# Kernel tuning notes

Hardware: AMD Instinct MI355X
Metric: run time of the kernel (lower is better)

The kernel has to match this reference:

```python
import jax, jax.numpy as jnp
import numpy as np

C = 512
CQK = C // 8  # 64


def setup_inputs() -> dict:
    key = jax.random.key(0)
    ks = jax.random.split(key, 8)
    B, H, W = 16, 32, 32
    x = jax.random.normal(ks[0], (B, C, H, W), dtype=jnp.float32)
    # 1x1 conv weights stored as [out_ch, in_ch] matrices + biases
    sq = 1.0 / np.sqrt(C)
    Wq = jax.random.uniform(ks[1], (CQK, C), jnp.float32, -sq, sq)
    bq = jax.random.uniform(ks[2], (CQK,), jnp.float32, -sq, sq)
    Wk = jax.random.uniform(ks[3], (CQK, C), jnp.float32, -sq, sq)
    bk = jax.random.uniform(ks[4], (CQK,), jnp.float32, -sq, sq)
    Wv = jax.random.uniform(ks[5], (C, C), jnp.float32, -sq, sq)
    bv = jax.random.uniform(ks[6], (C,), jnp.float32, -sq, sq)
    gamma = jax.random.normal(ks[7], (1,), dtype=jnp.float32)
    return {"x": x, "Wq": Wq, "bq": bq, "Wk": Wk, "bk": bk, "Wv": Wv, "bv": bv, "gamma": gamma}


def reference(x, Wq, bq, Wk, bk, Wv, bv, gamma):
    B, Cin, H, W = x.shape
    xf = x.reshape(B, Cin, H * W)  # [B, C, N]
    # 1x1 convs == channel matmuls
    q = jnp.einsum('qc,bcn->bnq', Wq, xf) + bq[None, None, :]   # [B, N, Cqk]
    k = jnp.einsum('qc,bcn->bqn', Wk, xf) + bk[None, :, None]   # [B, Cqk, N]
    v = jnp.einsum('vc,bcn->bvn', Wv, xf) + bv[None, :, None]   # [B, C, N]
    scores = jnp.einsum('bnq,bqm->bnm', q, k)                    # [B, N, N]
    attn = jax.nn.softmax(scores, axis=-1)                       # softmax over keys
    # values @ attn^T : out[b,c,n] = sum_m v[b,c,m] * attn[b,n,m]
    attended = jnp.einsum('bvm,bnm->bvn', v, attn)               # [B, C, N]
    attended = attended.reshape(B, Cin, H, W)
    return gamma[0] * attended + x
```

## Files before the change

### kernel.cpp

```cpp
#include <hip/hip_runtime.h>
#include <stdint.h>

#define BB 16
#define CC 512
#define CQK 64
#define NN 1024

typedef __attribute__((ext_vector_type(8))) short bf16x8;
typedef __attribute__((ext_vector_type(4))) short short4v;
typedef __attribute__((ext_vector_type(8))) unsigned short ushort8;
typedef __attribute__((ext_vector_type(4))) float f32x4;

static __device__ __forceinline__ unsigned short f2bf(float f) {
  uint32_t u = __float_as_uint(f);
  u += 0x7FFFu + ((u >> 16) & 1u);
  return (unsigned short)(u >> 16);
}

static __device__ __forceinline__ void gll16(const unsigned short* g, unsigned short* l) {
  const __attribute__((address_space(1))) unsigned int* gp =
      reinterpret_cast<const __attribute__((address_space(1))) unsigned int*>(
          reinterpret_cast<uintptr_t>(g));
  __attribute__((address_space(3))) unsigned int* lp =
      reinterpret_cast<__attribute__((address_space(3))) unsigned int*>(
          (unsigned int)reinterpret_cast<uintptr_t>(l));
  __builtin_amdgcn_global_load_lds(gp, lp, 16, 0, 0);
}

__global__ __launch_bounds__(256) void k_pack_w(
    const float* __restrict__ Wq, const float* __restrict__ Wk,
    const float* __restrict__ Wv, unsigned short* __restrict__ Wall) {
  int idx = blockIdx.x * 256 + threadIdx.x;
  int e = idx * 4;
  if (e >= 640 * 512) return;
  int o = e >> 9;
  int c = e & 511;
  const float* src;
  if (o < 64)        src = Wq + (size_t)o * 512;
  else if (o < 128)  src = Wk + (size_t)(o - 64) * 512;
  else               src = Wv + (size_t)(o - 128) * 512;
  float4 v = *(const float4*)(src + c);
  short4v pk;
  pk[0] = (short)f2bf(v.x); pk[1] = (short)f2bf(v.y);
  pk[2] = (short)f2bf(v.z); pk[3] = (short)f2bf(v.w);
  *(short4v*)(Wall + e) = pk;
}

__global__ __launch_bounds__(256) void k_transpose_x(
    const float* __restrict__ x, unsigned short* __restrict__ xT) {
  __shared__ float tile[32][33];
  int b = blockIdx.z;
  int c0 = blockIdx.y * 32;
  int n0 = blockIdx.x * 32;
  int t = threadIdx.x;
  int tn = t & 31, tc = t >> 5;
  const float* xp = x + ((size_t)b * CC + c0) * NN + n0;
#pragma unroll
  for (int i = 0; i < 4; i++) {
    int c = tc + i * 8;
    tile[c][tn] = xp[(size_t)c * NN + tn];
  }
  __syncthreads();
  unsigned short* xq = xT + ((size_t)b * NN + n0) * CC + c0;
  int n = t >> 3;
  int cq = (t & 7) * 4;
  short4v pk;
#pragma unroll
  for (int k = 0; k < 4; k++) pk[k] = (short)f2bf(tile[cq + k][n]);
  *(short4v*)(&xq[(size_t)n * CC + cq]) = pk;
}

__global__ __launch_bounds__(256) void k_gemm1(
    const unsigned short* __restrict__ Wall, const unsigned short* __restrict__ xT,
    const float* __restrict__ bq, const float* __restrict__ bk,
    const float* __restrict__ bv,
    unsigned short* __restrict__ qkT, unsigned short* __restrict__ vbuf) {
  __shared__ __align__(16) unsigned short ldsA[128 * 32];
  __shared__ __align__(16) unsigned short ldsB[128 * 32];
  int b = blockIdx.z;
  int o0 = blockIdx.y * 128;
  int n0 = blockIdx.x * 128;
  int t = threadIdx.x;
  int w = t >> 6, l = t & 63;
  int wm = w & 1, wn = w >> 1;
  int lr = l & 15, lq = l >> 4;

  f32x4 acc[4][4];
#pragma unroll
  for (int i = 0; i < 4; i++)
#pragma unroll
    for (int j = 0; j < 4; j++) acc[i][j] = (f32x4){0.f, 0.f, 0.f, 0.f};

  const unsigned short* Ab = Wall + (size_t)o0 * CC;
  const unsigned short* Bb = xT + ((size_t)b * NN + n0) * CC;
  int srow = t >> 2;
  int skq = (t & 3) * 8;
  int ldsw = (t >> 6) * 512;

  for (int kt = 0; kt < CC; kt += 32) {
#pragma unroll
    for (int p = 0; p < 2; p++) {
      int r = p * 64 + srow;
      gll16(&Ab[(size_t)r * CC + kt + skq], &ldsA[p * 2048 + ldsw]);
      gll16(&Bb[(size_t)r * CC + kt + skq], &ldsB[p * 2048 + ldsw]);
    }
    __syncthreads();
    bf16x8 af[4], bfr[4];
#pragma unroll
    for (int i = 0; i < 4; i++)
      af[i] = *(const bf16x8*)(&ldsA[(wm * 64 + i * 16 + lr) * 32 + lq * 8]);
#pragma unroll
    for (int j = 0; j < 4; j++)
      bfr[j] = *(const bf16x8*)(&ldsB[(wn * 64 + j * 16 + lr) * 32 + lq * 8]);
#pragma unroll
    for (int i = 0; i < 4; i++)
#pragma unroll
      for (int j = 0; j < 4; j++)
        acc[i][j] = __builtin_amdgcn_mfma_f32_16x16x32_bf16(af[i], bfr[j], acc[i][j], 0, 0, 0);
    __syncthreads();
  }

  if (o0 == 0) {
#pragma unroll
    for (int i = 0; i < 4; i++) {
      int ob = wm * 64 + i * 16 + lq * 4;
#pragma unroll
      for (int j = 0; j < 4; j++) {
        int n = n0 + wn * 64 + j * 16 + lr;
        short4v pk;
#pragma unroll
        for (int r = 0; r < 4; r++) {
          int o = ob + r;
          float bias = (o < 64) ? bq[o] : bk[o - 64];
          pk[r] = (short)f2bf(acc[i][j][r] + bias);
        }
        *(short4v*)(&qkT[((size_t)b * NN + n) * 128 + ob]) = pk;
      }
    }
  } else {
#pragma unroll
    for (int i = 0; i < 4; i++) {
#pragma unroll
      for (int r = 0; r < 4; r++) {
        int o = o0 + wm * 64 + i * 16 + lq * 4 + r;
        int c = o - 128;
        float bias = bv[c];
#pragma unroll
        for (int j = 0; j < 4; j++) {
          int n = n0 + wn * 64 + j * 16 + lr;
          vbuf[((size_t)b * CC + c) * NN + n] = f2bf(acc[i][j][r] + bias);
        }
      }
    }
  }
}

#define QT 64
#define MC 64
#define PSTR 72

__global__ __launch_bounds__(256, 4) void k_flash(
    const unsigned short* __restrict__ qkT, const unsigned short* __restrict__ vbuf,
    const float* __restrict__ x, const float* __restrict__ gamma,
    float* __restrict__ out) {
  __shared__ __align__(16) unsigned short P[2][QT * PSTR];
  __shared__ float red[4 * QT];
  __shared__ float fin[QT];

  int lin = blockIdx.x;
  int ntile = lin >> 6;
  int rem = lin & 63;
  int b = rem >> 2;
  int cq = rem & 3;
  int n0 = ntile * QT;
  int t = threadIdx.x;
  int w = t >> 6, l = t & 63;
  int lr = l & 15, lq = l >> 4;
  const unsigned short* qk = qkT + (size_t)b * NN * 128;
  const unsigned short* Vb = vbuf + ((size_t)b * CC + cq * 128 + w * 32) * NN;

  bf16x8 aq[4][2];
#pragma unroll
  for (int nj = 0; nj < 4; nj++)
#pragma unroll
    for (int ks = 0; ks < 2; ks++)
      aq[nj][ks] = *(const bf16x8*)(&qk[(size_t)(n0 + nj * 16 + lr) * 128 + ks * 32 + lq * 8]);

  f32x4 acc[2][4];
#pragma unroll
  for (int ci = 0; ci < 2; ci++)
#pragma unroll
    for (int nj = 0; nj < 4; nj++) acc[ci][nj] = (f32x4){0.f, 0.f, 0.f, 0.f};
  float sreg[4][4];
#pragma unroll
  for (int nj = 0; nj < 4; nj++)
#pragma unroll
    for (int r = 0; r < 4; r++) sreg[nj][r] = 0.f;

  float ev[4][4];
  {
    int mrow = w * 16 + lr;
    bf16x8 kf0 = *(const bf16x8*)(&qk[(size_t)mrow * 128 + 64 + lq * 8]);
    bf16x8 kf1 = *(const bf16x8*)(&qk[(size_t)mrow * 128 + 96 + lq * 8]);
#pragma unroll
    for (int nj = 0; nj < 4; nj++) {
      f32x4 s = (f32x4){0.f, 0.f, 0.f, 0.f};
      s = __builtin_amdgcn_mfma_f32_16x16x32_bf16(aq[nj][0], kf0, s, 0, 0, 0);
      s = __builtin_amdgcn_mfma_f32_16x16x32_bf16(aq[nj][1], kf1, s, 0, 0, 0);
#pragma unroll
      for (int r = 0; r < 4; r++) {
        float e = __expf(s[r]);
        ev[nj][r] = e;
        sreg[nj][r] += e;
      }
    }
  }

  for (int ch = 0; ch < NN / MC; ch++) {
    int m0 = ch * MC;
    unsigned short* Pb = P[ch & 1];
#pragma unroll
    for (int nj = 0; nj < 4; nj++)
#pragma unroll
      for (int r = 0; r < 4; r++)
        Pb[(nj * 16 + lq * 4 + r) * PSTR + w * 16 + lr] = f2bf(ev[nj][r]);

    if (ch + 1 < NN / MC) {
      int mrow = m0 + MC + w * 16 + lr;
      bf16x8 kf0 = *(const bf16x8*)(&qk[(size_t)mrow * 128 + 64 + lq * 8]);
      bf16x8 kf1 = *(const bf16x8*)(&qk[(size_t)mrow * 128 + 96 + lq * 8]);
#pragma unroll
      for (int nj = 0; nj < 4; nj++) {
        f32x4 s = (f32x4){0.f, 0.f, 0.f, 0.f};
        s = __builtin_amdgcn_mfma_f32_16x16x32_bf16(aq[nj][0], kf0, s, 0, 0, 0);
        s = __builtin_amdgcn_mfma_f32_16x16x32_bf16(aq[nj][1], kf1, s, 0, 0, 0);
#pragma unroll
        for (int r = 0; r < 4; r++) {
          float e = __expf(s[r]);
          ev[nj][r] = e;
          sreg[nj][r] += e;
        }
      }
    }

    bf16x8 af[2][2];
#pragma unroll
    for (int ci = 0; ci < 2; ci++)
#pragma unroll
      for (int ks = 0; ks < 2; ks++)
        af[ci][ks] = *(const bf16x8*)(&Vb[(size_t)(ci * 16 + lr) * NN + m0 + ks * 32 + lq * 8]);

    __syncthreads();

#pragma unroll
    for (int ks = 0; ks < 2; ks++)
#pragma unroll
      for (int nj = 0; nj < 4; nj++) {
        bf16x8 pf = *(const bf16x8*)(&Pb[(nj * 16 + lr) * PSTR + ks * 32 + lq * 8]);
#pragma unroll
        for (int ci = 0; ci < 2; ci++)
          acc[ci][nj] = __builtin_amdgcn_mfma_f32_16x16x32_bf16(af[ci][ks], pf, acc[ci][nj], 0, 0, 0);
      }
  }

#pragma unroll
  for (int nj = 0; nj < 4; nj++)
#pragma unroll
    for (int r = 0; r < 4; r++) {
#pragma unroll
      for (int d = 1; d < 16; d <<= 1) sreg[nj][r] += __shfl_xor(sreg[nj][r], d, 64);
    }
  __syncthreads();
  if (lr == 0) {
#pragma unroll
    for (int nj = 0; nj < 4; nj++)
#pragma unroll
      for (int r = 0; r < 4; r++) red[w * QT + nj * 16 + lq * 4 + r] = sreg[nj][r];
  }
  __syncthreads();
  if (t < QT) {
    fin[t] = red[t] + red[QT + t] + red[2 * QT + t] + red[3 * QT + t];
  }
  __syncthreads();

  float invL[4];
#pragma unroll
  for (int nj = 0; nj < 4; nj++) invL[nj] = 1.0f / fin[nj * 16 + lr];
  float g = gamma[0];
#pragma unroll
  for (int ci = 0; ci < 2; ci++) {
#pragma unroll
    for (int r = 0; r < 4; r++) {
      int c = cq * 128 + w * 32 + ci * 16 + lq * 4 + r;
#pragma unroll
      for (int nj = 0; nj < 4; nj++) {
        size_t idx = ((size_t)b * CC + c) * NN + n0 + nj * 16 + lr;
        out[idx] = g * acc[ci][nj][r] * invL[nj] + x[idx];
      }
    }
  }
}

extern "C" void kernel_launch(void* const* d_in, const int* in_sizes, int n_in,
                              void* d_out, int out_size, void* d_ws, size_t ws_size,
                              hipStream_t stream) {
  (void)in_sizes; (void)n_in; (void)out_size; (void)ws_size;
  const float* x     = (const float*)d_in[0];
  const float* Wq    = (const float*)d_in[1];
  const float* bq    = (const float*)d_in[2];
  const float* Wk    = (const float*)d_in[3];
  const float* bk    = (const float*)d_in[4];
  const float* Wv    = (const float*)d_in[5];
  const float* bv    = (const float*)d_in[6];
  const float* gamma = (const float*)d_in[7];
  float* out = (float*)d_out;

  char* ws = (char*)d_ws;
  unsigned short* Wall = (unsigned short*)(ws);
  unsigned short* xT   = (unsigned short*)(ws + 655360);
  unsigned short* qkT  = (unsigned short*)(ws + 655360 + 16777216);
  unsigned short* vbuf = (unsigned short*)(ws + 655360 + 16777216 + 4194304);

  k_pack_w<<<dim3(320), dim3(256), 0, stream>>>(Wq, Wk, Wv, Wall);
  k_transpose_x<<<dim3(NN / 32, CC / 32, BB), dim3(256), 0, stream>>>(x, xT);
  k_gemm1<<<dim3(NN / 128, 640 / 128, BB), dim3(256), 0, stream>>>(Wall, xT, bq, bk, bv, qkT, vbuf);
  k_flash<<<dim3((NN / QT) * 4 * BB), dim3(256), 0, stream>>>(qkT, vbuf, x, gamma, out);
}
```

Measured before the change: 184.0 us.

## Merge prep kernels and widen flash block to 512 threads over half channels

Merges the weight packing and x transpose into a single launch to cut one kernel launch. The flash kernel now uses 8 waves per block, each block covering half the channels instead of a quarter. It processes 128 keys per chunk, so each block computes scores for a query tile once for twice as many channels, halving redundant QK/softmax work. V loads are hoisted ahead of the next-chunk score computation. The trade-off is more registers and more LDS per block, plus fewer blocks in the grid.

```diff
diff --git a/kernel.cpp b/kernel.cpp
--- a/kernel.cpp
+++ b/kernel.cpp
@@ -27,47 +27,49 @@
   __builtin_amdgcn_global_load_lds(gp, lp, 16, 0, 0);
 }
 
-__global__ __launch_bounds__(256) void k_pack_w(
-    const float* __restrict__ Wq, const float* __restrict__ Wk,
-    const float* __restrict__ Wv, unsigned short* __restrict__ Wall) {
-  int idx = blockIdx.x * 256 + threadIdx.x;
-  int e = idx * 4;
-  if (e >= 640 * 512) return;
-  int o = e >> 9;
-  int c = e & 511;
-  const float* src;
-  if (o < 64)        src = Wq + (size_t)o * 512;
-  else if (o < 128)  src = Wk + (size_t)(o - 64) * 512;
-  else               src = Wv + (size_t)(o - 128) * 512;
-  float4 v = *(const float4*)(src + c);
-  short4v pk;
-  pk[0] = (short)f2bf(v.x); pk[1] = (short)f2bf(v.y);
-  pk[2] = (short)f2bf(v.z); pk[3] = (short)f2bf(v.w);
-  *(short4v*)(Wall + e) = pk;
-}
-
-__global__ __launch_bounds__(256) void k_transpose_x(
-    const float* __restrict__ x, unsigned short* __restrict__ xT) {
-  __shared__ float tile[32][33];
-  int b = blockIdx.z;
-  int c0 = blockIdx.y * 32;
-  int n0 = blockIdx.x * 32;
+__global__ __launch_bounds__(256) void k_prep(
+    const float* __restrict__ x, const float* __restrict__ Wq,
+    const float* __restrict__ Wk, const float* __restrict__ Wv,
+    unsigned short* __restrict__ xT, unsigned short* __restrict__ Wall) {
+  int blk = blockIdx.x;
   int t = threadIdx.x;
-  int tn = t & 31, tc = t >> 5;
-  const float* xp = x + ((size_t)b * CC + c0) * NN + n0;
-#pragma unroll
-  for (int i = 0; i < 4; i++) {
-    int c = tc + i * 8;
-    tile[c][tn] = xp[(size_t)c * NN + tn];
-  }
-  __syncthreads();
-  unsigned short* xq = xT + ((size_t)b * NN + n0) * CC + c0;
-  int n = t >> 3;
-  int cq = (t & 7) * 4;
-  short4v pk;
-#pragma unroll
-  for (int k = 0; k < 4; k++) pk[k] = (short)f2bf(tile[cq + k][n]);
-  *(short4v*)(&xq[(size_t)n * CC + cq]) = pk;
+  if (blk < 8192) {
+    __shared__ float tile[32][33];
+    int b = blk >> 9;
+    int rem = blk & 511;
+    int c0 = (rem >> 5) * 32;
+    int n0 = (rem & 31) * 32;
+    int tn = t & 31, tc = t >> 5;
+    const float* xp = x + ((size_t)b * CC + c0) * NN + n0;
+#pragma unroll
+    for (int i = 0; i < 4; i++) {
+      int c = tc + i * 8;
+      tile[c][tn] = xp[(size_t)c * NN + tn];
+    }
+    __syncthreads();
+    unsigned short* xq = xT + ((size_t)b * NN + n0) * CC + c0;
+    int n = t >> 3;
+    int cq = (t & 7) * 4;
+    short4v pk;
+#pragma unroll
+    for (int k = 0; k < 4; k++) pk[k] = (short)f2bf(tile[cq + k][n]);
+    *(short4v*)(&xq[(size_t)n * CC + cq]) = pk;
+  } else {
+    int idx = (blk - 8192) * 256 + t;
+    int e = idx * 4;
+    if (e >= 640 * 512) return;
+    int o = e >> 9;
+    int c = e & 511;
+    const float* src;
+    if (o < 64)        src = Wq + (size_t)o * 512;
+    else if (o < 128)  src = Wk + (size_t)(o - 64) * 512;
+    else               src = Wv + (size_t)(o - 128) * 512;
+    float4 v = *(const float4*)(src + c);
+    short4v pk;
+    pk[0] = (short)f2bf(v.x); pk[1] = (short)f2bf(v.y);
+    pk[2] = (short)f2bf(v.z); pk[3] = (short)f2bf(v.w);
+    *(short4v*)(Wall + e) = pk;
+  }
 }
 
 __global__ __launch_bounds__(256) void k_gemm1(
@@ -156,28 +158,28 @@
 }
 
 #define QT 64
-#define MC 64
-#define PSTR 72
-
-__global__ __launch_bounds__(256, 4) void k_flash(
+#define MC 128
+#define PSTR 136
+
+__global__ __launch_bounds__(512, 4) void k_flash(
     const unsigned short* __restrict__ qkT, const unsigned short* __restrict__ vbuf,
     const float* __restrict__ x, const float* __restrict__ gamma,
     float* __restrict__ out) {
   __shared__ __align__(16) unsigned short P[2][QT * PSTR];
-  __shared__ float red[4 * QT];
+  __shared__ float red[8 * QT];
   __shared__ float fin[QT];
 
   int lin = blockIdx.x;
-  int ntile = lin >> 6;
-  int rem = lin & 63;
-  int b = rem >> 2;
-  int cq = rem & 3;
+  int ntile = lin >> 5;
+  int rem = lin & 31;
+  int b = rem >> 1;
+  int chalf = rem & 1;
   int n0 = ntile * QT;
   int t = threadIdx.x;
   int w = t >> 6, l = t & 63;
   int lr = l & 15, lq = l >> 4;
   const unsigned short* qk = qkT + (size_t)b * NN * 128;
-  const unsigned short* Vb = vbuf + ((size_t)b * CC + cq * 128 + w * 32) * NN;
+  const unsigned short* Vb = vbuf + ((size_t)b * CC + chalf * 256 + w * 32) * NN;
 
   bf16x8 aq[4][2];
 #pragma unroll
@@ -225,15 +227,25 @@
       for (int r = 0; r < 4; r++)
         Pb[(nj * 16 + lq * 4 + r) * PSTR + w * 16 + lr] = f2bf(ev[nj][r]);
 
+    bf16x8 kf0n, kf1n;
     if (ch + 1 < NN / MC) {
       int mrow = m0 + MC + w * 16 + lr;
-      bf16x8 kf0 = *(const bf16x8*)(&qk[(size_t)mrow * 128 + 64 + lq * 8]);
-      bf16x8 kf1 = *(const bf16x8*)(&qk[(size_t)mrow * 128 + 96 + lq * 8]);
+      kf0n = *(const bf16x8*)(&qk[(size_t)mrow * 128 + 64 + lq * 8]);
+      kf1n = *(const bf16x8*)(&qk[(size_t)mrow * 128 + 96 + lq * 8]);
+    }
+    bf16x8 af[2][4];
+#pragma unroll
+    for (int ci = 0; ci < 2; ci++)
+#pragma unroll
+      for (int ks = 0; ks < 4; ks++)
+        af[ci][ks] = *(const bf16x8*)(&Vb[(size_t)(ci * 16 + lr) * NN + m0 + ks * 32 + lq * 8]);
+
+    if (ch + 1 < NN / MC) {
 #pragma unroll
       for (int nj = 0; nj < 4; nj++) {
         f32x4 s = (f32x4){0.f, 0.f, 0.f, 0.f};
-        s = __builtin_amdgcn_mfma_f32_16x16x32_bf16(aq[nj][0], kf0, s, 0, 0, 0);
-        s = __builtin_amdgcn_mfma_f32_16x16x32_bf16(aq[nj][1], kf1, s, 0, 0, 0);
+        s = __builtin_amdgcn_mfma_f32_16x16x32_bf16(aq[nj][0], kf0n, s, 0, 0, 0);
+        s = __builtin_amdgcn_mfma_f32_16x16x32_bf16(aq[nj][1], kf1n, s, 0, 0, 0);
 #pragma unroll
         for (int r = 0; r < 4; r++) {
           float e = __expf(s[r]);
@@ -243,17 +255,10 @@
       }
     }
 
-    bf16x8 af[2][2];
-#pragma unroll
-    for (int ci = 0; ci < 2; ci++)
-#pragma unroll
-      for (int ks = 0; ks < 2; ks++)
-        af[ci][ks] = *(const bf16x8*)(&Vb[(size_t)(ci * 16 + lr) * NN + m0 + ks * 32 + lq * 8]);
-
     __syncthreads();
 
 #pragma unroll
-    for (int ks = 0; ks < 2; ks++)
+    for (int ks = 0; ks < 4; ks++)
 #pragma unroll
       for (int nj = 0; nj < 4; nj++) {
         bf16x8 pf = *(const bf16x8*)(&Pb[(nj * 16 + lr) * PSTR + ks * 32 + lq * 8]);
@@ -279,7 +284,10 @@
   }
   __syncthreads();
   if (t < QT) {
-    fin[t] = red[t] + red[QT + t] + red[2 * QT + t] + red[3 * QT + t];
+    float ssum = 0.f;
+#pragma unroll
+    for (int ww = 0; ww < 8; ww++) ssum += red[ww * QT + t];
+    fin[t] = ssum;
   }
   __syncthreads();
 
@@ -291,7 +299,7 @@
   for (int ci = 0; ci < 2; ci++) {
 #pragma unroll
     for (int r = 0; r < 4; r++) {
-      int c = cq * 128 + w * 32 + ci * 16 + lq * 4 + r;
+      int c = chalf * 256 + w * 32 + ci * 16 + lq * 4 + r;
 #pragma unroll
       for (int nj = 0; nj < 4; nj++) {
         size_t idx = ((size_t)b * CC + c) * NN + n0 + nj * 16 + lr;
@@ -321,8 +329,7 @@
   unsigned short* qkT  = (unsigned short*)(ws + 655360 + 16777216);
   unsigned short* vbuf = (unsigned short*)(ws + 655360 + 16777216 + 4194304);
 
-  k_pack_w<<<dim3(320), dim3(256), 0, stream>>>(Wq, Wk, Wv, Wall);
-  k_transpose_x<<<dim3(NN / 32, CC / 32, BB), dim3(256), 0, stream>>>(x, xT);
+  k_prep<<<dim3(8512), dim3(256), 0, stream>>>(x, Wq, Wk, Wv, xT, Wall);
   k_gemm1<<<dim3(NN / 128, 640 / 128, BB), dim3(256), 0, stream>>>(Wall, xT, bq, bk, bv, qkT, vbuf);
-  k_flash<<<dim3((NN / QT) * 4 * BB), dim3(256), 0, stream>>>(qkT, vbuf, x, gamma, out);
-}
+  k_flash<<<dim3((NN / QT) * 2 * BB), dim3(512), 0, stream>>>(qkT, vbuf, x, gamma, out);
+}
```

Result: slower. 195.7 us (+6.4%).
